# Optimization experiments

Measured on AMD Instinct MI355X. Metric: run time of the kernel, lower is better.

## Reference

```python
import jax, jax.numpy as jnp
import numpy as np

NUM_HEADS = 16
ROPE_THETA = 10000.0


def apply_rope(x):
    # x: (B, H, T, hd), interleaved-pair RoPE (rotary-embedding-torch convention)
    T, hd = x.shape[-2], x.shape[-1]
    inv_freq = 1.0 / (ROPE_THETA ** (jnp.arange(0, hd, 2, dtype=jnp.float32) / hd))  # (hd/2,)
    ang = jnp.arange(T, dtype=jnp.float32)[:, None] * inv_freq[None, :]  # (T, hd/2)
    cos, sin = jnp.cos(ang), jnp.sin(ang)
    x1 = x[..., 0::2]
    x2 = x[..., 1::2]
    r1 = x1 * cos - x2 * sin
    r2 = x1 * sin + x2 * cos
    return jnp.stack([r1, r2], axis=-1).reshape(x.shape)


def setup_inputs() -> dict:
    key = jax.random.key(0)
    ks = jax.random.split(key, 8)
    L, S, B, E = 2048, 2048, 2, 1024
    sc = 1.0 / np.sqrt(E)
    return {
        "query": jax.random.normal(ks[0], (L, B, E), jnp.float32),
        "key": jax.random.normal(ks[1], (S, B, E), jnp.float32),
        "value": jax.random.normal(ks[2], (S, B, E), jnp.float32),
        "key_padding_mask": jnp.zeros((B, S), dtype=bool),
        "Wq": jax.random.normal(ks[3], (E, E), jnp.float32) * sc,
        "bq": jnp.zeros((E,), jnp.float32),
        "Wk": jax.random.normal(ks[4], (E, E), jnp.float32) * sc,
        "bk": jnp.zeros((E,), jnp.float32),
        "Wv": jax.random.normal(ks[5], (E, E), jnp.float32) * sc,
        "bv": jnp.zeros((E,), jnp.float32),
        "Wo": jax.random.normal(ks[6], (E, E), jnp.float32) * sc,
        "bo": jnp.zeros((E,), jnp.float32),
    }


def reference(query, key, value, key_padding_mask, Wq, bq, Wk, bk, Wv, bv, Wo, bo):
    L, B, E = query.shape
    S = key.shape[0]
    H = NUM_HEADS
    hd = E // H
    # projections (torch Linear: x @ W.T + b)
    Q = query @ Wq.T + bq  # (L, B, E)
    K = key @ Wk.T + bk    # (S, B, E)
    V = value @ Wv.T + bv  # (S, B, E)
    # (T, B, E) -> (B, H, T, hd)
    Q = Q.reshape(L, B, H, hd).transpose(1, 2, 0, 3)
    K = K.reshape(S, B, H, hd).transpose(1, 2, 0, 3)
    V = V.reshape(S, B, H, hd).transpose(1, 2, 0, 3)
    Q = apply_rope(Q)
    K = apply_rope(K)
    scores = jnp.einsum("bhld,bhsd->bhls", Q, K) / jnp.sqrt(jnp.float32(hd))
    scores = jnp.where(key_padding_mask[:, None, None, :], -jnp.inf, scores)
    attn = jax.nn.softmax(scores, axis=-1)
    out = jnp.einsum("bhls,bhsd->bhld", attn, V)  # (B, H, L, hd)
    out = out.transpose(2, 0, 1, 3).reshape(L, B, E)
    return out @ Wo.T + bo
```

## Files before the change

### kernel.cpp

```cpp
#include <hip/hip_runtime.h>
#include <hip/hip_bf16.h>

typedef __hip_bfloat16 bf16;
typedef short bf16x8 __attribute__((ext_vector_type(8)));
typedef float f32x4 __attribute__((ext_vector_type(4)));
typedef short s4 __attribute__((ext_vector_type(4)));

#define LL 2048
#define SS 2048
#define EE 1024
#define HH 16
#define HD 64
#define MM (LL * 2)

static __device__ __forceinline__ short f2bs(float f) {
  bf16 h = __float2bfloat16(f);
  short u;
  __builtin_memcpy(&u, &h, 2);
  return u;
}

static __device__ __forceinline__ void st8(bf16* p, float4 x, float4 y) {
  bf16x8 v;
  v[0] = f2bs(x.x); v[1] = f2bs(x.y); v[2] = f2bs(x.z); v[3] = f2bs(x.w);
  v[4] = f2bs(y.x); v[5] = f2bs(y.y); v[6] = f2bs(y.z); v[7] = f2bs(y.w);
  *(bf16x8*)p = v;
}

#define GLL16(gp, lp) __builtin_amdgcn_global_load_lds(                        \
    (const __attribute__((address_space(1))) void*)(gp),                       \
    (__attribute__((address_space(3))) void*)(lp), 16, 0, 0)

__global__ __launch_bounds__(256) void prep_kernel(
    float2* __restrict__ tab, const unsigned char* __restrict__ m,
    float* __restrict__ mf,
    const float* __restrict__ s0, const float* __restrict__ s1,
    const float* __restrict__ s2, const float* __restrict__ s3,
    bf16* __restrict__ wdst, float* __restrict__ zout) {
  const int bid = blockIdx.x;
  if (bid < 256) {
    int i = bid * 256 + threadIdx.x;
    int pos = i >> 5, fi = i & 31;
    float freq = expf(-(float)fi * (9.210340371976184f / 32.0f));
    float ang = (float)pos * freq;
    float s, c;
    sincosf(ang, &s, &c);
    tab[i] = make_float2(c, s);
  } else if (bid < 272) {
    int i = (bid - 256) * 256 + threadIdx.x;
    if (i < 2 * SS) mf[i] = m[i] ? -1e30f : 0.f;
  } else if (bid < 4368) {
    int b2 = bid - 272;
    int sel = b2 >> 10;
    const float* src = (sel == 0) ? s0 : (sel == 1) ? s1 : (sel == 2) ? s2 : s3;
    size_t loc = ((size_t)(b2 & 1023) * 256 + threadIdx.x) * 4;
    float4 v = *(const float4*)(src + loc);
    s4 p;
    p[0] = f2bs(v.x); p[1] = f2bs(v.y); p[2] = f2bs(v.z); p[3] = f2bs(v.w);
    *(s4*)(wdst + (size_t)sel * EE * EE + loc) = p;
  } else {
    size_t i = ((size_t)(bid - 4368) * 256 + threadIdx.x) * 4;
    *(float4*)(zout + i) = make_float4(0.f, 0.f, 0.f, 0.f);
  }
}

template<int MODE, bool XB16, bool WB16>
__global__ __launch_bounds__(256) void proj_kernel(
    const void* __restrict__ Xv, const void* __restrict__ Wv,
    const float* __restrict__ bias, void* __restrict__ dstv,
    const float2* __restrict__ tab)
{
  const int w = threadIdx.x >> 6;
  const int lane = threadIdx.x & 63;
  const int l15 = lane & 15, quad = lane >> 4;
  const int tm = blockIdx.x * 128 + w * 32;
  const int tn = blockIdx.y * 64;

  const size_t aoff0 = (size_t)(tm + l15) * EE + quad * 8;
  const size_t aoff1 = aoff0 + (size_t)16 * EE;
  const size_t woff  = (size_t)(tn + l15) * EE + quad * 8;

  f32x4 zero4 = {0.f, 0.f, 0.f, 0.f};
  f32x4 acc[2][4];
#pragma unroll
  for (int mi = 0; mi < 2; ++mi)
#pragma unroll
    for (int ni = 0; ni < 4; ++ni) acc[mi][ni] = zero4;

  for (int k0 = 0; k0 < EE; k0 += 32) {
    bf16x8 a0, a1;
    if (XB16 || MODE == 3) {
      const bf16* Xb = (const bf16*)Xv;
      a0 = *(const bf16x8*)(Xb + aoff0 + k0);
      a1 = *(const bf16x8*)(Xb + aoff1 + k0);
    } else {
      const float* Xf = (const float*)Xv;
#pragma unroll
      for (int j = 0; j < 8; ++j) a0[j] = f2bs(Xf[aoff0 + k0 + j]);
#pragma unroll
      for (int j = 0; j < 8; ++j) a1[j] = f2bs(Xf[aoff1 + k0 + j]);
    }
#pragma unroll
    for (int ni = 0; ni < 4; ++ni) {
      bf16x8 bv;
      if (WB16) {
        const bf16* Wb = (const bf16*)Wv;
        bv = *(const bf16x8*)(Wb + woff + (size_t)ni * 16 * EE + k0);
      } else {
        const float* Wf = (const float*)Wv;
#pragma unroll
        for (int j = 0; j < 8; ++j) bv[j] = f2bs(Wf[woff + (size_t)ni * 16 * EE + k0 + j]);
      }
      acc[0][ni] = __builtin_amdgcn_mfma_f32_16x16x32_bf16(a0, bv, acc[0][ni], 0, 0, 0);
      acc[1][ni] = __builtin_amdgcn_mfma_f32_16x16x32_bf16(a1, bv, acc[1][ni], 0, 0, 0);
    }
  }

  float bz[4];
#pragma unroll
  for (int ni = 0; ni < 4; ++ni) bz[ni] = bias[tn + ni * 16 + l15];

#pragma unroll
  for (int mi = 0; mi < 2; ++mi) {
#pragma unroll
    for (int ni = 0; ni < 4; ++ni) {
      const int n = tn + ni * 16 + l15;
#pragma unroll
      for (int r = 0; r < 4; ++r) {
        const int m = tm + mi * 16 + quad * 4 + r;
        float v = acc[mi][ni][r] + bz[ni];
        if (MODE <= 1) {
          float other = __shfl_xor(v, 1, 64);
          int pos = m >> 1, b = m & 1, d = n & 63, h = n >> 6;
          float2 cs = tab[pos * 32 + (d >> 1)];
          float rv = (d & 1) ? (other * cs.y + v * cs.x) : (v * cs.x - other * cs.y);
          ((bf16*)dstv)[((size_t)(b * HH + h) * LL + pos) * HD + d] = __float2bfloat16(rv);
        } else if (MODE == 2) {
          int pos = m >> 1, b = m & 1, d = n & 63, h = n >> 6;
          ((bf16*)dstv)[((size_t)(b * HH + h) * HD + d) * SS + pos] = __float2bfloat16(v);
        } else {
          ((float*)dstv)[(size_t)m * EE + n] = v;
        }
      }
    }
  }
}

__global__ __launch_bounds__(256, 6) void qkv_kernel(
    const float* __restrict__ Xq, const float* __restrict__ Xk,
    const float* __restrict__ Xv, const bf16* __restrict__ Wb,
    const float* __restrict__ bq, const float* __restrict__ bk,
    const float* __restrict__ bv, bf16* __restrict__ Qr,
    bf16* __restrict__ Kr, bf16* __restrict__ Vt,
    const float2* __restrict__ tab)
{
  __shared__ __align__(16) bf16 As[2][128 * 32];
  __shared__ __align__(16) bf16 Bs[2][64 * 32];

  const int tid = threadIdx.x;
  const int w = tid >> 6;
  const int lane = tid & 63;
  const int l15 = lane & 15, quad = lane >> 4;
  const int id = blockIdx.x;
  const int z = id >> 9;
  const int g = id & 511;
  const int tmb = (g & 31) * 128;
  const int tn  = (g >> 5) * 64;

  const float* Xf = (z == 0) ? Xq : (z == 1) ? Xk : Xv;
  const bf16* Wm  = Wb + (size_t)z * EE * EE;
  const float* bias = (z == 0) ? bq : (z == 1) ? bk : bv;
  bf16* dst = (z == 0) ? Qr : (z == 1) ? Kr : Vt;

  const int ar = tid >> 2;
  const int ac = (tid & 3) * 8;
  const float* gA0 = Xf + (size_t)(tmb + ar) * EE + ac;
  const float* gA1 = gA0 + (size_t)64 * EE;
  const bf16* gB = Wm + (size_t)(tn + w * 16 + (lane >> 2)) * EE + (lane & 3) * 8;

  f32x4 zero4 = {0.f, 0.f, 0.f, 0.f};
  f32x4 acc[2][4];
#pragma unroll
  for (int mi = 0; mi < 2; ++mi)
#pragma unroll
    for (int ni = 0; ni < 4; ++ni) acc[mi][ni] = zero4;

  {
    float4 a00 = *(const float4*)(gA0);
    float4 a01 = *(const float4*)(gA0 + 4);
    float4 a10 = *(const float4*)(gA1);
    float4 a11 = *(const float4*)(gA1 + 4);
    GLL16(gB, (bf16*)&Bs[0][w * 16 * 32] + lane * 8);
    st8(&As[0][ar * 32 + ac], a00, a01);
    st8(&As[0][(64 + ar) * 32 + ac], a10, a11);
  }
  __syncthreads();

  for (int t = 0; t < 32; ++t) {
    const int cur = t & 1;
    float4 a00, a01, a10, a11;
    if (t < 31) {
      const int k0 = (t + 1) * 32;
      a00 = *(const float4*)(gA0 + k0);
      a01 = *(const float4*)(gA0 + k0 + 4);
      a10 = *(const float4*)(gA1 + k0);
      a11 = *(const float4*)(gA1 + k0 + 4);
      GLL16(gB + k0, (bf16*)&Bs[cur ^ 1][w * 16 * 32] + lane * 8);
    }
    bf16x8 af0 = *(const bf16x8*)(&As[cur][(w * 32 + l15) * 32 + quad * 8]);
    bf16x8 af1 = *(const bf16x8*)(&As[cur][(w * 32 + 16 + l15) * 32 + quad * 8]);
#pragma unroll
    for (int ni = 0; ni < 4; ++ni) {
      bf16x8 bfr = *(const bf16x8*)(&Bs[cur][(ni * 16 + l15) * 32 + quad * 8]);
      acc[0][ni] = __builtin_amdgcn_mfma_f32_16x16x32_bf16(af0, bfr, acc[0][ni], 0, 0, 0);
      acc[1][ni] = __builtin_amdgcn_mfma_f32_16x16x32_bf16(af1, bfr, acc[1][ni], 0, 0, 0);
    }
    if (t < 31) {
      st8(&As[cur ^ 1][ar * 32 + ac], a00, a01);
      st8(&As[cur ^ 1][(64 + ar) * 32 + ac], a10, a11);
    }
    __syncthreads();
  }

  float bz[4];
#pragma unroll
  for (int ni = 0; ni < 4; ++ni) bz[ni] = bias[tn + ni * 16 + l15];

#pragma unroll
  for (int mi = 0; mi < 2; ++mi) {
#pragma unroll
    for (int ni = 0; ni < 4; ++ni) {
      const int n = tn + ni * 16 + l15;
#pragma unroll
      for (int r = 0; r < 4; ++r) {
        const int m = tmb + w * 32 + mi * 16 + quad * 4 + r;
        float v = acc[mi][ni][r] + bz[ni];
        if (z <= 1) {
          float other = __shfl_xor(v, 1, 64);
          int pos = m >> 1, b = m & 1, d = n & 63, h = n >> 6;
          float2 cs = tab[pos * 32 + (d >> 1)];
          float rv = (d & 1) ? (other * cs.y + v * cs.x) : (v * cs.x - other * cs.y);
          dst[((size_t)(b * HH + h) * LL + pos) * HD + d] = __float2bfloat16(rv);
        } else {
          int pos = m >> 1, b = m & 1, d = n & 63, h = n >> 6;
          dst[((size_t)(b * HH + h) * HD + d) * SS + pos] = __float2bfloat16(v);
        }
      }
    }
  }
}

__global__ __launch_bounds__(256, 8) void projo_kernel(
    const bf16* __restrict__ X, const bf16* __restrict__ W,
    const float* __restrict__ bias, float* __restrict__ dst)
{
  __shared__ __align__(16) bf16 As[2][64 * 32];
  __shared__ __align__(16) bf16 Bs[2][64 * 32];

  const int tid = threadIdx.x;
  const int w = tid >> 6;
  const int lane = tid & 63;
  const int l15 = lane & 15, quad = lane >> 4;
  const int tmb = blockIdx.x * 64;
  const int tn  = blockIdx.y * 64;
  const int kb  = blockIdx.z * 512;

  const bf16* gA = X + (size_t)(tmb + w * 16 + (lane >> 2)) * EE + kb + (lane & 3) * 8;
  const bf16* gB = W + (size_t)(tn  + w * 16 + (lane >> 2)) * EE + kb + (lane & 3) * 8;

  f32x4 zero4 = {0.f, 0.f, 0.f, 0.f};
  f32x4 acc[4];
#pragma unroll
  for (int ni = 0; ni < 4; ++ni) acc[ni] = zero4;

  GLL16(gA, (bf16*)&As[0][w * 16 * 32] + lane * 8);
  GLL16(gB, (bf16*)&Bs[0][w * 16 * 32] + lane * 8);
  __syncthreads();

  for (int t = 0; t < 16; ++t) {
    const int cur = t & 1;
    if (t < 15) {
      const int k0 = (t + 1) * 32;
      GLL16(gA + k0, (bf16*)&As[cur ^ 1][w * 16 * 32] + lane * 8);
      GLL16(gB + k0, (bf16*)&Bs[cur ^ 1][w * 16 * 32] + lane * 8);
    }
    bf16x8 af = *(const bf16x8*)(&As[cur][(w * 16 + l15) * 32 + quad * 8]);
#pragma unroll
    for (int ni = 0; ni < 4; ++ni) {
      bf16x8 bfr = *(const bf16x8*)(&Bs[cur][(ni * 16 + l15) * 32 + quad * 8]);
      acc[ni] = __builtin_amdgcn_mfma_f32_16x16x32_bf16(af, bfr, acc[ni], 0, 0, 0);
    }
    __syncthreads();
  }

  float bz[4];
#pragma unroll
  for (int ni = 0; ni < 4; ++ni)
    bz[ni] = (blockIdx.z == 0) ? bias[tn + ni * 16 + l15] : 0.f;

#pragma unroll
  for (int ni = 0; ni < 4; ++ni) {
    const int n = tn + ni * 16 + l15;
#pragma unroll
    for (int r = 0; r < 4; ++r) {
      const int m = tmb + w * 16 + quad * 4 + r;
      atomicAdd(&dst[(size_t)m * EE + n], acc[ni][r] + bz[ni]);
    }
  }
}

__global__ __launch_bounds__(256) void attn_kernel(
    const bf16* __restrict__ Qr, const bf16* __restrict__ Kr,
    const bf16* __restrict__ Vt, const float* __restrict__ maskf,
    bf16* __restrict__ ctx)
{
  __shared__ __align__(16) bf16 Ks[2][64 * 64];
  __shared__ __align__(16) bf16 Vs[2][64 * 64];
  __shared__ __align__(16) short Plds[4][32][56];

  const int w = threadIdx.x >> 6;
  const int lane = threadIdx.x & 63;
  const int l15 = lane & 15, quad = lane >> 4;
  const int id = blockIdx.x;
  const int bh = id & 31;
  const int qt = id >> 5;
  const int b = bh >> 4, h = bh & 15;
  const int q0 = qt * 128 + w * 32;

  const bf16* Qbh = Qr + (size_t)bh * LL * HD;
  const bf16* Kbh = Kr + (size_t)bh * SS * HD;
  const bf16* Vbh = Vt + (size_t)bh * HD * SS;
  const float* mrow = maskf + b * SS;

  bf16x8 qf[2][2];
#pragma unroll
  for (int mi = 0; mi < 2; ++mi) {
    const bf16* qp = Qbh + (size_t)(q0 + mi * 16 + l15) * HD + quad * 8;
    qf[mi][0] = *(const bf16x8*)(qp);
    qf[mi][1] = *(const bf16x8*)(qp + 32);
  }

  const int srow = lane >> 3;
  const int gswz = ((lane & 7) ^ srow) * 8;
  const int kswz0 = ((quad    ) ^ (l15 & 7)) * 8;
  const int kswz1 = ((quad + 4) ^ (l15 & 7)) * 8;

#define STAGE(buf, S0) {                                                       \
    _Pragma("unroll")                                                          \
    for (int i = 0; i < 2; ++i) {                                              \
      const int rb = w * 16 + i * 8;                                           \
      GLL16(Kbh + (size_t)((S0) + rb + srow) * HD + gswz,                      \
            (bf16*)&Ks[buf][rb * 64] + lane * 8);                              \
      GLL16(Vbh + (size_t)(rb + srow) * SS + (S0) + gswz,                      \
            (bf16*)&Vs[buf][rb * 64] + lane * 8);                              \
    }                                                                          \
  }

  f32x4 zero4 = {0.f, 0.f, 0.f, 0.f};
  f32x4 o[2][4];
#pragma unroll
  for (int mi = 0; mi < 2; ++mi)
#pragma unroll
    for (int t = 0; t < 4; ++t) o[mi][t] = zero4;
  float ps0 = 0.f, ps1 = 0.f;

  STAGE(0, 0);
  __syncthreads();

  for (int t = 0; t < SS / 64; ++t) {
    const int s0 = t * 64;
    const int cur = t & 1;
    if (t + 1 < SS / 64) STAGE(cur ^ 1, s0 + 64);

#pragma unroll
    for (int ss = 0; ss < 2; ++ss) {
      const bf16* Kb = &Ks[cur][ss * 32 * 64];
      bf16x8 kf00 = *(const bf16x8*)(Kb + (l15)      * 64 + kswz0);
      bf16x8 kf01 = *(const bf16x8*)(Kb + (l15)      * 64 + kswz1);
      bf16x8 kf10 = *(const bf16x8*)(Kb + (16 + l15) * 64 + kswz0);
      bf16x8 kf11 = *(const bf16x8*)(Kb + (16 + l15) * 64 + kswz1);
      bf16x8 vf[4];
#pragma unroll
      for (int tt = 0; tt < 4; ++tt)
        vf[tt] = *(const bf16x8*)(&Vs[cur][0] + (tt * 16 + l15) * 64 +
                                  (((ss * 4 + quad) ^ (l15 & 7)) * 8));
      f32x4 mv0 = *(const f32x4*)(mrow + s0 + ss * 32 + quad * 4);
      f32x4 mv1 = *(const f32x4*)(mrow + s0 + ss * 32 + 16 + quad * 4);

#pragma unroll
      for (int mi = 0; mi < 2; ++mi) {
        f32x4 sc0 = zero4, sc1 = zero4;
        sc0 = __builtin_amdgcn_mfma_f32_16x16x32_bf16(kf00, qf[mi][0], sc0, 0, 0, 0);
        sc0 = __builtin_amdgcn_mfma_f32_16x16x32_bf16(kf01, qf[mi][1], sc0, 0, 0, 0);
        sc1 = __builtin_amdgcn_mfma_f32_16x16x32_bf16(kf10, qf[mi][0], sc1, 0, 0, 0);
        sc1 = __builtin_amdgcn_mfma_f32_16x16x32_bf16(kf11, qf[mi][1], sc1, 0, 0, 0);
        s4 pk0, pk1;
#pragma unroll
        for (int r = 0; r < 4; ++r) {
          float p = __expf(sc0[r] * 0.125f + mv0[r]);
          if (mi == 0) ps0 += p; else ps1 += p;
          pk0[r] = f2bs(p);
        }
#pragma unroll
        for (int r = 0; r < 4; ++r) {
          float p = __expf(sc1[r] * 0.125f + mv1[r]);
          if (mi == 0) ps0 += p; else ps1 += p;
          pk1[r] = f2bs(p);
        }
        *(s4*)&Plds[w][mi * 16 + l15][quad * 4] = pk0;
        *(s4*)&Plds[w][mi * 16 + l15][16 + quad * 4] = pk1;
      }
      asm volatile("" ::: "memory");
      bf16x8 pf0 = *(const bf16x8*)&Plds[w][l15][quad * 8];
      bf16x8 pf1 = *(const bf16x8*)&Plds[w][16 + l15][quad * 8];
#pragma unroll
      for (int tt = 0; tt < 4; ++tt) {
        o[0][tt] = __builtin_amdgcn_mfma_f32_16x16x32_bf16(pf0, vf[tt], o[0][tt], 0, 0, 0);
        o[1][tt] = __builtin_amdgcn_mfma_f32_16x16x32_bf16(pf1, vf[tt], o[1][tt], 0, 0, 0);
      }
      asm volatile("" ::: "memory");
    }
    __syncthreads();
  }
#undef STAGE

  float lv0 = ps0; lv0 += __shfl_xor(lv0, 16, 64); lv0 += __shfl_xor(lv0, 32, 64);
  float lv1 = ps1; lv1 += __shfl_xor(lv1, 16, 64); lv1 += __shfl_xor(lv1, 32, 64);

#pragma unroll
  for (int mi = 0; mi < 2; ++mi) {
#pragma unroll
    for (int r = 0; r < 4; ++r) {
      float lv = (mi == 0) ? lv0 : lv1;
      float li = __shfl(lv, quad * 4 + r, 64);
      float inv = 1.0f / li;
      int q = q0 + mi * 16 + quad * 4 + r;
#pragma unroll
      for (int t = 0; t < 4; ++t) {
        float val = o[mi][t][r] * inv;
        ctx[(size_t)(q * 2 + b) * EE + (size_t)h * 64 + t * 16 + l15] = __float2bfloat16(val);
      }
    }
  }
}

extern "C" void kernel_launch(void* const* d_in, const int* in_sizes, int n_in,
                              void* d_out, int out_size, void* d_ws, size_t ws_size,
                              hipStream_t stream) {
  const float* query = (const float*)d_in[0];
  const float* key   = (const float*)d_in[1];
  const float* value = (const float*)d_in[2];
  const unsigned char* mask = (const unsigned char*)d_in[3];
  const float* Wq = (const float*)d_in[4];
  const float* bq = (const float*)d_in[5];
  const float* Wk = (const float*)d_in[6];
  const float* bk = (const float*)d_in[7];
  const float* Wv = (const float*)d_in[8];
  const float* bv = (const float*)d_in[9];
  const float* Wo = (const float*)d_in[10];
  const float* bo = (const float*)d_in[11];

  char* ws = (char*)d_ws;
  const bool big = ws_size >= ((size_t)41 << 20);

  float2* tab   = (float2*)ws;
  float*  maskf = (float*)(ws + (512 << 10));
  bf16* Wb = (bf16*)(ws + ((size_t)1 << 20));
  size_t base = big ? ((size_t)9 << 20) : ((size_t)1 << 20);
  bf16* Qr  = (bf16*)(ws + base);
  bf16* Kr  = (bf16*)(ws + base + ((size_t)8 << 20));
  bf16* Vt  = (bf16*)(ws + base + ((size_t)16 << 20));
  bf16* ctx = (bf16*)(ws + base + ((size_t)24 << 20));

  prep_kernel<<<big ? 8464 : 272, 256, 0, stream>>>(
      tab, mask, maskf, Wq, Wk, Wv, Wo, Wb, (float*)d_out);

  if (big) {
    qkv_kernel<<<1536, 256, 0, stream>>>(query, key, value, Wb, bq, bk, bv,
                                         Qr, Kr, Vt, tab);
  } else {
    dim3 gp(MM / 128, EE / 64);
    proj_kernel<0, false, false><<<gp, 256, 0, stream>>>(query, Wq, bq, Qr, tab);
    proj_kernel<1, false, false><<<gp, 256, 0, stream>>>(key,   Wk, bk, Kr, tab);
    proj_kernel<2, false, false><<<gp, 256, 0, stream>>>(value, Wv, bv, Vt, tab);
  }

  attn_kernel<<<(LL / 128) * 2 * HH, 256, 0, stream>>>(Qr, Kr, Vt, maskf, ctx);

  if (big) {
    dim3 go(MM / 64, EE / 64, 2);
    projo_kernel<<<go, 256, 0, stream>>>(ctx, Wb + (size_t)3 * EE * EE, bo, (float*)d_out);
  } else {
    dim3 gp(MM / 128, EE / 64);
    proj_kernel<3, true, false><<<gp, 256, 0, stream>>>(ctx, Wo, bo, d_out, tab);
  }
}
```

Before: 277.5 us.

## Swizzle LDS tiles, drop split-K atomics in out-proj, halve attention query tile

Three independent changes land together. The QKV and output-projection kernels get an XOR-swizzled LDS layout for the A and B tiles, meant to avoid LDS bank conflicts. The output projection moves from 2-way split-K with atomicAdd onto a zeroed output to a 128-row tile over the full K with direct stores, so prep_kernel no longer zeroes the output. The attention kernel drops from 32 to 16 query rows per wave, doubling the grid and setting a min-blocks occupancy hint, which trades K/V reuse per block for more parallelism and lower register pressure.

```diff
diff --git a/kernel.cpp b/kernel.cpp
--- a/kernel.cpp
+++ b/kernel.cpp
@@ -36,7 +36,7 @@
     float* __restrict__ mf,
     const float* __restrict__ s0, const float* __restrict__ s1,
     const float* __restrict__ s2, const float* __restrict__ s3,
-    bf16* __restrict__ wdst, float* __restrict__ zout) {
+    bf16* __restrict__ wdst) {
   const int bid = blockIdx.x;
   if (bid < 256) {
     int i = bid * 256 + threadIdx.x;
@@ -49,7 +49,7 @@
   } else if (bid < 272) {
     int i = (bid - 256) * 256 + threadIdx.x;
     if (i < 2 * SS) mf[i] = m[i] ? -1e30f : 0.f;
-  } else if (bid < 4368) {
+  } else {
     int b2 = bid - 272;
     int sel = b2 >> 10;
     const float* src = (sel == 0) ? s0 : (sel == 1) ? s1 : (sel == 2) ? s2 : s3;
@@ -58,9 +58,6 @@
     s4 p;
     p[0] = f2bs(v.x); p[1] = f2bs(v.y); p[2] = f2bs(v.z); p[3] = f2bs(v.w);
     *(s4*)(wdst + (size_t)sel * EE * EE + loc) = p;
-  } else {
-    size_t i = ((size_t)(bid - 4368) * 256 + threadIdx.x) * 4;
-    *(float4*)(zout + i) = make_float4(0.f, 0.f, 0.f, 0.f);
   }
 }
 
@@ -154,8 +151,8 @@
     bf16* __restrict__ Kr, bf16* __restrict__ Vt,
     const float2* __restrict__ tab)
 {
-  __shared__ __align__(16) bf16 As[2][128 * 32];
-  __shared__ __align__(16) bf16 Bs[2][64 * 32];
+  __shared__ __align__(16) bf16 As[2][4096];
+  __shared__ __align__(16) bf16 Bs[2][2048];
 
   const int tid = threadIdx.x;
   const int w = tid >> 6;
@@ -173,10 +170,17 @@
   bf16* dst = (z == 0) ? Qr : (z == 1) ? Kr : Vt;
 
   const int ar = tid >> 2;
-  const int ac = (tid & 3) * 8;
-  const float* gA0 = Xf + (size_t)(tmb + ar) * EE + ac;
+  const int akc = tid & 3;
+  const float* gA0 = Xf + (size_t)(tmb + ar) * EE + akc * 8;
   const float* gA1 = gA0 + (size_t)64 * EE;
-  const bf16* gB = Wm + (size_t)(tn + w * 16 + (lane >> 2)) * EE + (lane & 3) * 8;
+  const int aw0 = (ar >> 1) * 64 + (((((ar & 1) << 2) | akc) ^ ((ar >> 1) & 7)) * 8);
+  const int aw1 = aw0 + 2048;
+
+  const int ub = (lane & 7) ^ (lane >> 3);
+  const bf16* gB = Wm + (size_t)(tn + w * 16 + 2 * (lane >> 3) + (ub >> 2)) * EE
+                      + (ub & 3) * 8;
+
+  const int arbase = (l15 >> 1) * 64 + (((((l15 & 1) << 2) | quad) ^ (l15 >> 1)) * 8);
 
   f32x4 zero4 = {0.f, 0.f, 0.f, 0.f};
   f32x4 acc[2][4];
@@ -190,9 +194,9 @@
     float4 a01 = *(const float4*)(gA0 + 4);
     float4 a10 = *(const float4*)(gA1);
     float4 a11 = *(const float4*)(gA1 + 4);
-    GLL16(gB, (bf16*)&Bs[0][w * 16 * 32] + lane * 8);
-    st8(&As[0][ar * 32 + ac], a00, a01);
-    st8(&As[0][(64 + ar) * 32 + ac], a10, a11);
+    GLL16(gB, (bf16*)&Bs[0][w * 512] + lane * 8);
+    st8(&As[0][aw0], a00, a01);
+    st8(&As[0][aw1], a10, a11);
   }
   __syncthreads();
 
@@ -205,19 +209,19 @@
       a01 = *(const float4*)(gA0 + k0 + 4);
       a10 = *(const float4*)(gA1 + k0);
       a11 = *(const float4*)(gA1 + k0 + 4);
-      GLL16(gB + k0, (bf16*)&Bs[cur ^ 1][w * 16 * 32] + lane * 8);
-    }
-    bf16x8 af0 = *(const bf16x8*)(&As[cur][(w * 32 + l15) * 32 + quad * 8]);
-    bf16x8 af1 = *(const bf16x8*)(&As[cur][(w * 32 + 16 + l15) * 32 + quad * 8]);
+      GLL16(gB + k0, (bf16*)&Bs[cur ^ 1][w * 512] + lane * 8);
+    }
+    bf16x8 af0 = *(const bf16x8*)(&As[cur][w * 1024 + arbase]);
+    bf16x8 af1 = *(const bf16x8*)(&As[cur][w * 1024 + 512 + arbase]);
 #pragma unroll
     for (int ni = 0; ni < 4; ++ni) {
-      bf16x8 bfr = *(const bf16x8*)(&Bs[cur][(ni * 16 + l15) * 32 + quad * 8]);
+      bf16x8 bfr = *(const bf16x8*)(&Bs[cur][ni * 512 + arbase]);
       acc[0][ni] = __builtin_amdgcn_mfma_f32_16x16x32_bf16(af0, bfr, acc[0][ni], 0, 0, 0);
       acc[1][ni] = __builtin_amdgcn_mfma_f32_16x16x32_bf16(af1, bfr, acc[1][ni], 0, 0, 0);
     }
     if (t < 31) {
-      st8(&As[cur ^ 1][ar * 32 + ac], a00, a01);
-      st8(&As[cur ^ 1][(64 + ar) * 32 + ac], a10, a11);
+      st8(&As[cur ^ 1][aw0], a00, a01);
+      st8(&As[cur ^ 1][aw1], a10, a11);
     }
     __syncthreads();
   }
@@ -250,73 +254,86 @@
   }
 }
 
-__global__ __launch_bounds__(256, 8) void projo_kernel(
+__global__ __launch_bounds__(256) void projo_kernel(
     const bf16* __restrict__ X, const bf16* __restrict__ W,
     const float* __restrict__ bias, float* __restrict__ dst)
 {
-  __shared__ __align__(16) bf16 As[2][64 * 32];
-  __shared__ __align__(16) bf16 Bs[2][64 * 32];
+  __shared__ __align__(16) bf16 As[2][4096];
+  __shared__ __align__(16) bf16 Bs[2][2048];
 
   const int tid = threadIdx.x;
   const int w = tid >> 6;
   const int lane = tid & 63;
   const int l15 = lane & 15, quad = lane >> 4;
-  const int tmb = blockIdx.x * 64;
+  const int tmb = blockIdx.x * 128;
   const int tn  = blockIdx.y * 64;
-  const int kb  = blockIdx.z * 512;
-
-  const bf16* gA = X + (size_t)(tmb + w * 16 + (lane >> 2)) * EE + kb + (lane & 3) * 8;
-  const bf16* gB = W + (size_t)(tn  + w * 16 + (lane >> 2)) * EE + kb + (lane & 3) * 8;
+
+  const int ub = (lane & 7) ^ (lane >> 3);
+  const bf16* gA0 = X + (size_t)(tmb + w * 32 + 2 * (lane >> 3) + (ub >> 2)) * EE
+                       + (ub & 3) * 8;
+  const bf16* gA1 = gA0 + (size_t)16 * EE;
+  const bf16* gB  = W + (size_t)(tn + w * 16 + 2 * (lane >> 3) + (ub >> 2)) * EE
+                       + (ub & 3) * 8;
+
+  const int arbase = (l15 >> 1) * 64 + (((((l15 & 1) << 2) | quad) ^ (l15 >> 1)) * 8);
 
   f32x4 zero4 = {0.f, 0.f, 0.f, 0.f};
-  f32x4 acc[4];
-#pragma unroll
-  for (int ni = 0; ni < 4; ++ni) acc[ni] = zero4;
-
-  GLL16(gA, (bf16*)&As[0][w * 16 * 32] + lane * 8);
-  GLL16(gB, (bf16*)&Bs[0][w * 16 * 32] + lane * 8);
+  f32x4 acc[2][4];
+#pragma unroll
+  for (int mi = 0; mi < 2; ++mi)
+#pragma unroll
+    for (int ni = 0; ni < 4; ++ni) acc[mi][ni] = zero4;
+
+  GLL16(gA0, (bf16*)&As[0][w * 1024] + lane * 8);
+  GLL16(gA1, (bf16*)&As[0][w * 1024 + 512] + lane * 8);
+  GLL16(gB,  (bf16*)&Bs[0][w * 512] + lane * 8);
   __syncthreads();
 
-  for (int t = 0; t < 16; ++t) {
+  for (int t = 0; t < 32; ++t) {
     const int cur = t & 1;
-    if (t < 15) {
+    if (t < 31) {
       const int k0 = (t + 1) * 32;
-      GLL16(gA + k0, (bf16*)&As[cur ^ 1][w * 16 * 32] + lane * 8);
-      GLL16(gB + k0, (bf16*)&Bs[cur ^ 1][w * 16 * 32] + lane * 8);
-    }
-    bf16x8 af = *(const bf16x8*)(&As[cur][(w * 16 + l15) * 32 + quad * 8]);
+      GLL16(gA0 + k0, (bf16*)&As[cur ^ 1][w * 1024] + lane * 8);
+      GLL16(gA1 + k0, (bf16*)&As[cur ^ 1][w * 1024 + 512] + lane * 8);
+      GLL16(gB + k0,  (bf16*)&Bs[cur ^ 1][w * 512] + lane * 8);
+    }
+    bf16x8 af0 = *(const bf16x8*)(&As[cur][w * 1024 + arbase]);
+    bf16x8 af1 = *(const bf16x8*)(&As[cur][w * 1024 + 512 + arbase]);
 #pragma unroll
     for (int ni = 0; ni < 4; ++ni) {
-      bf16x8 bfr = *(const bf16x8*)(&Bs[cur][(ni * 16 + l15) * 32 + quad * 8]);
-      acc[ni] = __builtin_amdgcn_mfma_f32_16x16x32_bf16(af, bfr, acc[ni], 0, 0, 0);
+      bf16x8 bfr = *(const bf16x8*)(&Bs[cur][ni * 512 + arbase]);
+      acc[0][ni] = __builtin_amdgcn_mfma_f32_16x16x32_bf16(af0, bfr, acc[0][ni], 0, 0, 0);
+      acc[1][ni] = __builtin_amdgcn_mfma_f32_16x16x32_bf16(af1, bfr, acc[1][ni], 0, 0, 0);
     }
     __syncthreads();
   }
 
   float bz[4];
 #pragma unroll
-  for (int ni = 0; ni < 4; ++ni)
-    bz[ni] = (blockIdx.z == 0) ? bias[tn + ni * 16 + l15] : 0.f;
-
-#pragma unroll
-  for (int ni = 0; ni < 4; ++ni) {
-    const int n = tn + ni * 16 + l15;
-#pragma unroll
-    for (int r = 0; r < 4; ++r) {
-      const int m = tmb + w * 16 + quad * 4 + r;
-      atomicAdd(&dst[(size_t)m * EE + n], acc[ni][r] + bz[ni]);
-    }
-  }
-}
-
-__global__ __launch_bounds__(256) void attn_kernel(
+  for (int ni = 0; ni < 4; ++ni) bz[ni] = bias[tn + ni * 16 + l15];
+
+#pragma unroll
+  for (int mi = 0; mi < 2; ++mi) {
+#pragma unroll
+    for (int ni = 0; ni < 4; ++ni) {
+      const int n = tn + ni * 16 + l15;
+#pragma unroll
+      for (int r = 0; r < 4; ++r) {
+        const int m = tmb + w * 32 + mi * 16 + quad * 4 + r;
+        dst[(size_t)m * EE + n] = acc[mi][ni][r] + bz[ni];
+      }
+    }
+  }
+}
+
+__global__ __launch_bounds__(256, 4) void attn_kernel(
     const bf16* __restrict__ Qr, const bf16* __restrict__ Kr,
     const bf16* __restrict__ Vt, const float* __restrict__ maskf,
     bf16* __restrict__ ctx)
 {
   __shared__ __align__(16) bf16 Ks[2][64 * 64];
   __shared__ __align__(16) bf16 Vs[2][64 * 64];
-  __shared__ __align__(16) short Plds[4][32][56];
+  __shared__ __align__(16) short Plds[4][16][56];
 
   const int w = threadIdx.x >> 6;
   const int lane = threadIdx.x & 63;
@@ -325,19 +342,18 @@
   const int bh = id & 31;
   const int qt = id >> 5;
   const int b = bh >> 4, h = bh & 15;
-  const int q0 = qt * 128 + w * 32;
+  const int q0 = qt * 64 + w * 16;
 
   const bf16* Qbh = Qr + (size_t)bh * LL * HD;
   const bf16* Kbh = Kr + (size_t)bh * SS * HD;
   const bf16* Vbh = Vt + (size_t)bh * HD * SS;
   const float* mrow = maskf + b * SS;
 
-  bf16x8 qf[2][2];
-#pragma unroll
-  for (int mi = 0; mi < 2; ++mi) {
-    const bf16* qp = Qbh + (size_t)(q0 + mi * 16 + l15) * HD + quad * 8;
-    qf[mi][0] = *(const bf16x8*)(qp);
-    qf[mi][1] = *(const bf16x8*)(qp + 32);
+  bf16x8 qf0, qf1;
+  {
+    const bf16* qp = Qbh + (size_t)(q0 + l15) * HD + quad * 8;
+    qf0 = *(const bf16x8*)(qp);
+    qf1 = *(const bf16x8*)(qp + 32);
   }
 
   const int srow = lane >> 3;
@@ -357,12 +373,10 @@
   }
 
   f32x4 zero4 = {0.f, 0.f, 0.f, 0.f};
-  f32x4 o[2][4];
-#pragma unroll
-  for (int mi = 0; mi < 2; ++mi)
-#pragma unroll
-    for (int t = 0; t < 4; ++t) o[mi][t] = zero4;
-  float ps0 = 0.f, ps1 = 0.f;
+  f32x4 o[4];
+#pragma unroll
+  for (int t = 0; t < 4; ++t) o[t] = zero4;
+  float ps = 0.f;
 
   STAGE(0, 0);
   __syncthreads();
@@ -387,59 +401,48 @@
       f32x4 mv0 = *(const f32x4*)(mrow + s0 + ss * 32 + quad * 4);
       f32x4 mv1 = *(const f32x4*)(mrow + s0 + ss * 32 + 16 + quad * 4);
 
-#pragma unroll
-      for (int mi = 0; mi < 2; ++mi) {
-        f32x4 sc0 = zero4, sc1 = zero4;
-        sc0 = __builtin_amdgcn_mfma_f32_16x16x32_bf16(kf00, qf[mi][0], sc0, 0, 0, 0);
-        sc0 = __builtin_amdgcn_mfma_f32_16x16x32_bf16(kf01, qf[mi][1], sc0, 0, 0, 0);
-        sc1 = __builtin_amdgcn_mfma_f32_16x16x32_bf16(kf10, qf[mi][0], sc1, 0, 0, 0);
-        sc1 = __builtin_amdgcn_mfma_f32_16x16x32_bf16(kf11, qf[mi][1], sc1, 0, 0, 0);
-        s4 pk0, pk1;
-#pragma unroll
-        for (int r = 0; r < 4; ++r) {
-          float p = __expf(sc0[r] * 0.125f + mv0[r]);
-          if (mi == 0) ps0 += p; else ps1 += p;
-          pk0[r] = f2bs(p);
-        }
-#pragma unroll
-        for (int r = 0; r < 4; ++r) {
-          float p = __expf(sc1[r] * 0.125f + mv1[r]);
-          if (mi == 0) ps0 += p; else ps1 += p;
-          pk1[r] = f2bs(p);
-        }
-        *(s4*)&Plds[w][mi * 16 + l15][quad * 4] = pk0;
-        *(s4*)&Plds[w][mi * 16 + l15][16 + quad * 4] = pk1;
+      f32x4 sc0 = zero4, sc1 = zero4;
+      sc0 = __builtin_amdgcn_mfma_f32_16x16x32_bf16(kf00, qf0, sc0, 0, 0, 0);
+      sc0 = __builtin_amdgcn_mfma_f32_16x16x32_bf16(kf01, qf1, sc0, 0, 0, 0);
+      sc1 = __builtin_amdgcn_mfma_f32_16x16x32_bf16(kf10, qf0, sc1, 0, 0, 0);
+      sc1 = __builtin_amdgcn_mfma_f32_16x16x32_bf16(kf11, qf1, sc1, 0, 0, 0);
+      s4 pk0, pk1;
+#pragma unroll
+      for (int r = 0; r < 4; ++r) {
+        float p = __expf(sc0[r] * 0.125f + mv0[r]);
+        ps += p; pk0[r] = f2bs(p);
       }
+#pragma unroll
+      for (int r = 0; r < 4; ++r) {
+        float p = __expf(sc1[r] * 0.125f + mv1[r]);
+        ps += p; pk1[r] = f2bs(p);
+      }
+      *(s4*)&Plds[w][l15][quad * 4] = pk0;
+      *(s4*)&Plds[w][l15][16 + quad * 4] = pk1;
       asm volatile("" ::: "memory");
-      bf16x8 pf0 = *(const bf16x8*)&Plds[w][l15][quad * 8];
-      bf16x8 pf1 = *(const bf16x8*)&Plds[w][16 + l15][quad * 8];
-#pragma unroll
-      for (int tt = 0; tt < 4; ++tt) {
-        o[0][tt] = __builtin_amdgcn_mfma_f32_16x16x32_bf16(pf0, vf[tt], o[0][tt], 0, 0, 0);
-        o[1][tt] = __builtin_amdgcn_mfma_f32_16x16x32_bf16(pf1, vf[tt], o[1][tt], 0, 0, 0);
-      }
+      bf16x8 pf = *(const bf16x8*)&Plds[w][l15][quad * 8];
+#pragma unroll
+      for (int tt = 0; tt < 4; ++tt)
+        o[tt] = __builtin_amdgcn_mfma_f32_16x16x32_bf16(pf, vf[tt], o[tt], 0, 0, 0);
       asm volatile("" ::: "memory");
     }
     __syncthreads();
   }
 #undef STAGE
 
-  float lv0 = ps0; lv0 += __shfl_xor(lv0, 16, 64); lv0 += __shfl_xor(lv0, 32, 64);
-  float lv1 = ps1; lv1 += __shfl_xor(lv1, 16, 64); lv1 += __shfl_xor(lv1, 32, 64);
-
-#pragma unroll
-  for (int mi = 0; mi < 2; ++mi) {
-#pragma unroll
-    for (int r = 0; r < 4; ++r) {
-      float lv = (mi == 0) ? lv0 : lv1;
-      float li = __shfl(lv, quad * 4 + r, 64);
-      float inv = 1.0f / li;
-      int q = q0 + mi * 16 + quad * 4 + r;
-#pragma unroll
-      for (int t = 0; t < 4; ++t) {
-        float val = o[mi][t][r] * inv;
-        ctx[(size_t)(q * 2 + b) * EE + (size_t)h * 64 + t * 16 + l15] = __float2bfloat16(val);
-      }
+  float lv = ps;
+  lv += __shfl_xor(lv, 16, 64);
+  lv += __shfl_xor(lv, 32, 64);
+
+#pragma unroll
+  for (int r = 0; r < 4; ++r) {
+    float li = __shfl(lv, quad * 4 + r, 64);
+    float inv = 1.0f / li;
+    int q = q0 + quad * 4 + r;
+#pragma unroll
+    for (int t = 0; t < 4; ++t) {
+      float val = o[t][r] * inv;
+      ctx[(size_t)(q * 2 + b) * EE + (size_t)h * 64 + t * 16 + l15] = __float2bfloat16(val);
     }
   }
 }
@@ -472,8 +475,8 @@
   bf16* Vt  = (bf16*)(ws + base + ((size_t)16 << 20));
   bf16* ctx = (bf16*)(ws + base + ((size_t)24 << 20));
 
-  prep_kernel<<<big ? 8464 : 272, 256, 0, stream>>>(
-      tab, mask, maskf, Wq, Wk, Wv, Wo, Wb, (float*)d_out);
+  prep_kernel<<<big ? 4368 : 272, 256, 0, stream>>>(
+      tab, mask, maskf, Wq, Wk, Wv, Wo, Wb);
 
   if (big) {
     qkv_kernel<<<1536, 256, 0, stream>>>(query, key, value, Wb, bq, bk, bv,
@@ -485,10 +488,10 @@
     proj_kernel<2, false, false><<<gp, 256, 0, stream>>>(value, Wv, bv, Vt, tab);
   }
 
-  attn_kernel<<<(LL / 128) * 2 * HH, 256, 0, stream>>>(Qr, Kr, Vt, maskf, ctx);
+  attn_kernel<<<(LL / 64) * 2 * HH, 256, 0, stream>>>(Qr, Kr, Vt, maskf, ctx);
 
   if (big) {
-    dim3 go(MM / 64, EE / 64, 2);
+    dim3 go(MM / 128, EE / 64);
     projo_kernel<<<go, 256, 0, stream>>>(ctx, Wb + (size_t)3 * EE * EE, bo, (float*)d_out);
   } else {
     dim3 gp(MM / 128, EE / 64);
```

Result: faster. 251.6 us (-9.3%).
